# Kernel tuning notes

Hardware: AMD Instinct MI355X
Metric: run time of the kernel (lower is better)

Reference implementation:

```python
import jax, jax.numpy as jnp
import numpy as np

EMBED = 1024
DMODEL = 1024
NHEAD = 16
HEAD = DMODEL // NHEAD  # 64
EPS = 1e-5


def layer_norm(x, g, b):
    mu = jnp.mean(x, axis=-1, keepdims=True)
    var = jnp.var(x, axis=-1, keepdims=True)
    return (x - mu) / jnp.sqrt(var + EPS) * g + b


def setup_inputs() -> dict:
    key = jax.random.key(0)
    ks = jax.random.split(key, 16)
    s = 0.02
    B, T = 2, 2048
    return {
        "x": jax.random.normal(ks[0], (B, T, EMBED), jnp.float32),
        "wq": jax.random.normal(ks[1], (NHEAD, EMBED, HEAD), jnp.float32) * s,
        "bq": jnp.zeros((NHEAD, HEAD), jnp.float32),
        "wk": jax.random.normal(ks[2], (NHEAD, EMBED, HEAD), jnp.float32) * s,
        "bk": jnp.zeros((NHEAD, HEAD), jnp.float32),
        "wv": jax.random.normal(ks[3], (NHEAD, EMBED, HEAD), jnp.float32) * s,
        "bv": jnp.zeros((NHEAD, HEAD), jnp.float32),
        "ln1_g": jnp.ones((EMBED,), jnp.float32),
        "ln1_b": jnp.zeros((EMBED,), jnp.float32),
        "ln2_g": jnp.ones((DMODEL,), jnp.float32),
        "ln2_b": jnp.zeros((DMODEL,), jnp.float32),
        "w1": jax.random.normal(ks[4], (DMODEL, 4 * DMODEL), jnp.float32) * s,
        "b1": jnp.zeros((4 * DMODEL,), jnp.float32),
        "w2": jax.random.normal(ks[5], (4 * DMODEL, EMBED), jnp.float32) * s,
        "b2": jnp.zeros((EMBED,), jnp.float32),
    }


def reference(x, wq, bq, wk, bk, wv, bv, ln1_g, ln1_b, ln2_g, ln2_b, w1, b1, w2, b2):
    B, T, C = x.shape
    h = layer_norm(x, ln1_g, ln1_b)  # note: residual uses the normalized x (as in source)
    # per-head projections, vectorized over heads: [B,H,T,D]
    q = jnp.einsum('btc,hcd->bhtd', h, wq) + bq[None, :, None, :]
    k = jnp.einsum('btc,hcd->bhtd', h, wk) + bk[None, :, None, :]
    v = jnp.einsum('btc,hcd->bhtd', h, wv) + bv[None, :, None, :]
    scores = jnp.einsum('bhtd,bhsd->bhts', q, k) / jnp.sqrt(jnp.float32(HEAD))
    causal = jnp.tril(jnp.ones((T, T), bool))
    scores = jnp.where(causal[None, None], scores, jnp.finfo(scores.dtype).min)
    wei = jax.nn.softmax(scores, axis=-1)
    attn = jnp.einsum('bhts,bhsd->bhtd', wei, v)
    attn = attn.transpose(0, 2, 1, 3).reshape(B, T, NHEAD * HEAD)  # concat heads
    y = h + attn
    z = layer_norm(y, ln2_g, ln2_b)
    ff = jax.nn.relu(z @ w1 + b1) @ w2 + b2
    return z + ff
```

## Files before the change

kernel.cpp:

```cpp
#include <hip/hip_runtime.h>
#include <hip/hip_bf16.h>
#include <cstdint>
#include <cstddef>

typedef __attribute__((ext_vector_type(8))) short bf16x8;
typedef __attribute__((ext_vector_type(4))) float f32x4;
typedef __attribute__((ext_vector_type(4))) short short4v;
typedef __attribute__((ext_vector_type(2))) unsigned int uint2v;

__device__ inline void gload_lds16(const void* g, void* l) {
  __builtin_amdgcn_global_load_lds((const __attribute__((address_space(1))) void*)g,
                                   (__attribute__((address_space(3))) void*)l, 16, 0, 0);
}

__device__ inline float exp2_fast(float x) {
  float r;
  asm volatile("v_exp_f32 %0, %1" : "=v"(r) : "v"(x));
  return r;
}

__device__ inline unsigned int cvt_pk_bf16(float lo, float hi) {
  unsigned int r;
  asm volatile("v_cvt_pk_bf16_f32 %0, %1, %2" : "=v"(r) : "v"(lo), "v"(hi));
  return r;
}

__global__ void transpose_pack(const float* __restrict__ src, __hip_bfloat16* __restrict__ dst,
                               int R, int C, int ldDst, long zSrcStride, int zDstRow)
{
  __shared__ float tile[64][65];
  src += (size_t)blockIdx.z * zSrcStride;
  const int r0 = blockIdx.y * 64, c0 = blockIdx.x * 64;
  const int t = threadIdx.x;
#pragma unroll
  for (int i = 0; i < 16; ++i) {
    int idx = i * 256 + t;
    int r = idx >> 6, c = idx & 63;
    tile[r][c] = src[(size_t)(r0 + r) * C + c0 + c];
  }
  __syncthreads();
  const int drow0 = blockIdx.z * zDstRow + c0;
#pragma unroll
  for (int i = 0; i < 16; ++i) {
    int idx = i * 256 + t;
    int cc = idx >> 6, rr = idx & 63;
    dst[(size_t)(drow0 + cc) * ldDst + r0 + rr] = __float2bfloat16(tile[rr][cc]);
  }
}

__global__ void ln_fused(const float* __restrict__ x, const float* __restrict__ add,
                         const float* __restrict__ g, const float* __restrict__ bta,
                         float* __restrict__ of32, __hip_bfloat16* __restrict__ obf)
{
  const int row = blockIdx.x;
  const int t = threadIdx.x;
  float4 v = ((const float4*)(x + (size_t)row * 1024))[t];
  if (add) {
    float4 a = ((const float4*)(add + (size_t)row * 1024))[t];
    v.x += a.x; v.y += a.y; v.z += a.z; v.w += a.w;
  }
  float s = v.x + v.y + v.z + v.w;
  float ss = v.x * v.x + v.y * v.y + v.z * v.z + v.w * v.w;
#pragma unroll
  for (int off = 1; off < 64; off <<= 1) {
    s += __shfl_xor(s, off);
    ss += __shfl_xor(ss, off);
  }
  __shared__ float sb[4], ssb[4];
  const int w = t >> 6, lane = t & 63;
  if (lane == 0) { sb[w] = s; ssb[w] = ss; }
  __syncthreads();
  s = sb[0] + sb[1] + sb[2] + sb[3];
  ss = ssb[0] + ssb[1] + ssb[2] + ssb[3];
  const float mu = s * (1.f / 1024.f);
  const float var = ss * (1.f / 1024.f) - mu * mu;
  const float rstd = rsqrtf(var + 1e-5f);
  float4 gv = ((const float4*)g)[t];
  float4 bv = ((const float4*)bta)[t];
  float4 o;
  o.x = (v.x - mu) * rstd * gv.x + bv.x;
  o.y = (v.y - mu) * rstd * gv.y + bv.y;
  o.z = (v.z - mu) * rstd * gv.z + bv.z;
  o.w = (v.w - mu) * rstd * gv.w + bv.w;
  ((float4*)(of32 + (size_t)row * 1024))[t] = o;
  __hip_bfloat16 hb[4] = { __float2bfloat16(o.x), __float2bfloat16(o.y),
                           __float2bfloat16(o.z), __float2bfloat16(o.w) };
  *(short4v*)(obf + (size_t)row * 1024 + t * 4) = *(const short4v*)hb;
}

template<int EPI>
__global__ __launch_bounds__(512, 2) void gemm_bt(
    const __hip_bfloat16* __restrict__ A, const __hip_bfloat16* __restrict__ Bt,
    int N, int Kf, int kLen,
    const float* __restrict__ bias,
    const float* __restrict__ bq, const float* __restrict__ bk, const float* __restrict__ bv,
    __hip_bfloat16* __restrict__ oq, __hip_bfloat16* __restrict__ ok, __hip_bfloat16* __restrict__ ovt,
    __hip_bfloat16* __restrict__ obf,
    float* __restrict__ opart0, float* __restrict__ opart1, float* __restrict__ opart2)
{
  __shared__ short As[2][128 * 32];
  __shared__ short Bs[2][256 * 32];
  const int t = threadIdx.x;
  const int lane = t & 63;
  const int w = t >> 6;
  const int wm = w >> 2, wn = w & 3;
  const int l15 = lane & 15, lg = lane >> 4;
  const int m0 = blockIdx.y * 128;
  const int n0 = blockIdx.x * 256;
  const int kBase = (EPI == 2) ? (int)blockIdx.z * kLen : 0;
  const int kEnd0 = kBase + kLen;
  const int kEnd = (kEnd0 > Kf) ? Kf : kEnd0;

  f32x4 acc[4][4];
#pragma unroll
  for (int i = 0; i < 4; ++i)
#pragma unroll
    for (int j = 0; j < 4; ++j)
#pragma unroll
      for (int e = 0; e < 4; ++e) acc[i][j][e] = 0.f;

  auto STAGE = [&](int buf, int kk0) {
    {
      const int r = t >> 2, cc = t & 3;
      const int kk = (cc ^ ((r >> 1) & 3)) * 8;
      gload_lds16(A + (size_t)(m0 + r) * Kf + kk0 + kk, (char*)As + buf * 8192 + t * 16);
    }
#pragma unroll
    for (int i = 0; i < 2; ++i) {
      const int c = t + 512 * i;
      const int r = c >> 2, cc = c & 3;
      const int kk = (cc ^ ((r >> 1) & 3)) * 8;
      gload_lds16(Bt + (size_t)(n0 + r) * Kf + kk0 + kk, (char*)Bs + buf * 16384 + c * 16);
    }
  };

  STAGE(0, kBase);
  int buf = 0;
  for (int k0 = kBase; k0 < kEnd; k0 += 32) {
    const int knext = (k0 + 32 < kEnd) ? k0 + 32 : k0;
    STAGE(buf ^ 1, knext);
    asm volatile("s_waitcnt vmcnt(3)" ::: "memory");
    __builtin_amdgcn_s_barrier();
    asm volatile("" ::: "memory");

    bf16x8 af[4], bfr[4];
#pragma unroll
    for (int fm = 0; fm < 4; ++fm) {
      const int r = wm * 64 + fm * 16 + l15;
      const int kc = lg ^ ((r >> 1) & 3);
      af[fm] = *(const bf16x8*)&As[buf][r * 32 + kc * 8];
    }
#pragma unroll
    for (int fn = 0; fn < 4; ++fn) {
      const int r = wn * 64 + fn * 16 + l15;
      const int kc = lg ^ ((r >> 1) & 3);
      bfr[fn] = *(const bf16x8*)&Bs[buf][r * 32 + kc * 8];
    }
#pragma unroll
    for (int fm = 0; fm < 4; ++fm)
#pragma unroll
      for (int fn = 0; fn < 4; ++fn)
        acc[fm][fn] = __builtin_amdgcn_mfma_f32_16x16x32_bf16(af[fm], bfr[fn], acc[fm][fn], 0, 0, 0);

    asm volatile("" ::: "memory");
    __builtin_amdgcn_s_barrier();
    buf ^= 1;
  }

#pragma unroll
  for (int fm = 0; fm < 4; ++fm) {
    const int mbase = m0 + wm * 64 + fm * 16 + lg * 4;
#pragma unroll
    for (int fn = 0; fn < 4; ++fn) {
      const int n = n0 + wn * 64 + fn * 16 + l15;
      if (EPI == 0) {
        const int seg = n >> 10;
        const int cn = n & 1023;
        const int h = cn >> 6, d = cn & 63;
        const float* bp = (seg == 0) ? bq : (seg == 1) ? bk : bv;
        const float bias_v = bp[cn];
#pragma unroll
        for (int rg = 0; rg < 4; ++rg) {
          const int m = mbase + rg;
          const int b = m >> 11, tt = m & 2047;
          const size_t bh = (size_t)(b * 16 + h);
          const float val = acc[fm][fn][rg] + bias_v;
          if (seg == 0)      oq[(bh * 2048 + tt) * 64 + d] = __float2bfloat16(val);
          else if (seg == 1) ok[(bh * 2048 + tt) * 64 + d] = __float2bfloat16(val);
          else               ovt[(bh * 64 + d) * 2048 + tt] = __float2bfloat16(val);
        }
      } else if (EPI == 1) {
        const float bias_v = bias[n];
#pragma unroll
        for (int rg = 0; rg < 4; ++rg) {
          const int m = mbase + rg;
          float val = acc[fm][fn][rg] + bias_v;
          val = fmaxf(val, 0.f);
          obf[(size_t)m * N + n] = __float2bfloat16(val);
        }
      } else {
        float* op = (blockIdx.z == 0) ? opart0 : (blockIdx.z == 1) ? opart1 : opart2;
#pragma unroll
        for (int rg = 0; rg < 4; ++rg) {
          const int m = mbase + rg;
          op[(size_t)m * 1024 + n] = acc[fm][fn][rg];
        }
      }
    }
  }
}

__global__ void ffn2_merge(const float* __restrict__ p0, const float* __restrict__ p1,
                           const float* __restrict__ p2,
                           const float* __restrict__ z, const float* __restrict__ b2,
                           float* __restrict__ out)
{
  const size_t i = ((size_t)blockIdx.x * 256 + threadIdx.x) * 4;
  const float4 a = *(const float4*)(p0 + i);
  const float4 b = *(const float4*)(p1 + i);
  const float4 d = *(const float4*)(p2 + i);
  const float4 c = *(const float4*)(z + i);
  const float4 bb = *(const float4*)(b2 + (i & 1023));
  float4 o;
  o.x = c.x + bb.x + a.x + b.x + d.x;
  o.y = c.y + bb.y + a.y + b.y + d.y;
  o.z = c.z + bb.z + a.z + b.z + d.z;
  o.w = c.w + bb.w + a.w + b.w + d.w;
  *(float4*)(out + i) = o;
}

__global__ __launch_bounds__(256, 3) void flash_attn(
    const __hip_bfloat16* __restrict__ Q, const __hip_bfloat16* __restrict__ Kb,
    const __hip_bfloat16* __restrict__ Vt,
    __hip_bfloat16* __restrict__ Opart, float* __restrict__ Lpart)
{
  __shared__ short Ks[2][64 * 64];
  __shared__ short Vs[2][64 * 64];
  __shared__ short P2[4][32 * 72];
  const int t = threadIdx.x;
  const int lane = t & 63, w = t >> 6;
  const int l15 = lane & 15, lg = lane >> 4;
  const int chunk = blockIdx.x, qblk = blockIdx.y, bh = blockIdx.z;
  const int q0 = qblk * 128;
  const int s_base = chunk * 512;
  if (s_base > q0 + 127) return;
  const int s_hi = (s_base + 512 < q0 + 128) ? s_base + 512 : q0 + 128;
  const int ntiles = (s_hi - s_base) >> 6;
  const int qw = q0 + w * 32;

  const __hip_bfloat16* Qbh = Q + (size_t)bh * 2048 * 64;
  const __hip_bfloat16* Kbh = Kb + (size_t)bh * 2048 * 64;
  const __hip_bfloat16* Vbh = Vt + (size_t)bh * 64 * 2048;

  bf16x8 qf[2][2];
#pragma unroll
  for (int fm = 0; fm < 2; ++fm)
#pragma unroll
    for (int kc = 0; kc < 2; ++kc)
      qf[fm][kc] = *(const bf16x8*)(Qbh + (size_t)(qw + fm * 16 + l15) * 64 + kc * 32 + lg * 8);

  const int srow = (w << 4) + (lane >> 3);
  const int schunk = ((lane & 7) ^ (lane >> 3)) * 8;

  auto STAGE = [&](int bufi, int s0) {
#pragma unroll
    for (int i = 0; i < 2; ++i) {
      const int r = srow + i * 8;
      const int dst = bufi * 8192 + w * 2048 + i * 1024 + lane * 16;
      gload_lds16(Kbh + (size_t)(s0 + r) * 64 + schunk, (char*)Ks + dst);
      gload_lds16(Vbh + (size_t)r * 2048 + s0 + schunk, (char*)Vs + dst);
    }
  };

  f32x4 o_acc[2][4];
  float lpart[2] = {0.f, 0.f};
#pragma unroll
  for (int fm = 0; fm < 2; ++fm)
#pragma unroll
    for (int fd = 0; fd < 4; ++fd)
#pragma unroll
      for (int e = 0; e < 4; ++e) o_acc[fm][fd][e] = 0.f;

  const float C = 0.18033688011112042f;

  STAGE(0, s_base);
  int cur = 0;
  for (int ti = 0; ti < ntiles; ++ti) {
    const int s0 = s_base + ti * 64;
    const int nxt = (ti + 1 < ntiles) ? s0 + 64 : s0;
    STAGE(cur ^ 1, nxt);
    asm volatile("s_waitcnt vmcnt(4)" ::: "memory");
    __builtin_amdgcn_s_barrier();
    asm volatile("" ::: "memory");

    if (s0 <= qw + 31) {
      f32x4 s_acc[2][4];
#pragma unroll
      for (int fm = 0; fm < 2; ++fm)
#pragma unroll
        for (int fn = 0; fn < 4; ++fn)
#pragma unroll
          for (int e = 0; e < 4; ++e) s_acc[fm][fn][e] = 0.f;
#pragma unroll
      for (int kc = 0; kc < 2; ++kc)
#pragma unroll
        for (int fn = 0; fn < 4; ++fn) {
          const int r = fn * 16 + l15;
          bf16x8 kf = *(const bf16x8*)&Ks[cur][r * 64 + ((((kc << 2) | lg) ^ (l15 & 7)) << 3)];
          s_acc[0][fn] = __builtin_amdgcn_mfma_f32_16x16x32_bf16(kf, qf[0][kc], s_acc[0][fn], 0, 0, 0);
          s_acc[1][fn] = __builtin_amdgcn_mfma_f32_16x16x32_bf16(kf, qf[1][kc], s_acc[1][fn], 0, 0, 0);
        }

      const bool needmask = (s0 + 63 > qw);
      float pr[2][4][4];
#pragma unroll
      for (int fm = 0; fm < 2; ++fm) {
        const int qv = qw + fm * 16 + l15;
#pragma unroll
        for (int fn = 0; fn < 4; ++fn)
#pragma unroll
          for (int rg = 0; rg < 4; ++rg) {
            float p = exp2_fast(s_acc[fm][fn][rg] * C);
            if (needmask) {
              const int sg = s0 + fn * 16 + lg * 4 + rg;
              p = (sg <= qv) ? p : 0.f;
            }
            pr[fm][fn][rg] = p;
            lpart[fm] += p;
          }
      }

#pragma unroll
      for (int fm = 0; fm < 2; ++fm)
#pragma unroll
        for (int fn = 0; fn < 4; ++fn) {
          uint2v u;
          u.x = cvt_pk_bf16(pr[fm][fn][0], pr[fm][fn][1]);
          u.y = cvt_pk_bf16(pr[fm][fn][2], pr[fm][fn][3]);
          *(uint2v*)&P2[w][(fm * 16 + l15) * 72 + fn * 16 + lg * 4] = u;
        }

#pragma unroll
      for (int kc = 0; kc < 2; ++kc) {
        bf16x8 pf0 = *(const bf16x8*)&P2[w][(l15) * 72 + kc * 32 + lg * 8];
        bf16x8 pf1 = *(const bf16x8*)&P2[w][(16 + l15) * 72 + kc * 32 + lg * 8];
#pragma unroll
        for (int fd = 0; fd < 4; ++fd) {
          const int r = fd * 16 + l15;
          bf16x8 vf = *(const bf16x8*)&Vs[cur][r * 64 + ((((kc << 2) | lg) ^ (l15 & 7)) << 3)];
          o_acc[0][fd] = __builtin_amdgcn_mfma_f32_16x16x32_bf16(vf, pf0, o_acc[0][fd], 0, 0, 0);
          o_acc[1][fd] = __builtin_amdgcn_mfma_f32_16x16x32_bf16(vf, pf1, o_acc[1][fd], 0, 0, 0);
        }
      }
    }

    asm volatile("" ::: "memory");
    __builtin_amdgcn_s_barrier();
    cur ^= 1;
  }

  const int pslot = ((bh * 16 + qblk) << 2) + chunk;
  __hip_bfloat16* op = Opart + (size_t)pslot * 8192;
#pragma unroll
  for (int fm = 0; fm < 2; ++fm) {
    float l = lpart[fm];
    l += __shfl_xor(l, 16);
    l += __shfl_xor(l, 32);
    const int qloc = w * 32 + fm * 16 + l15;
    if (lg == 0) Lpart[pslot * 128 + qloc] = l;
#pragma unroll
    for (int fd = 0; fd < 4; ++fd) {
      uint2v u;
      u.x = cvt_pk_bf16(o_acc[fm][fd][0], o_acc[fm][fd][1]);
      u.y = cvt_pk_bf16(o_acc[fm][fd][2], o_acc[fm][fd][3]);
      *(uint2v*)(op + (size_t)qloc * 64 + fd * 16 + lg * 4) = u;
    }
  }
}

__global__ void flash_merge(const __hip_bfloat16* __restrict__ Opart,
                            const float* __restrict__ Lpart, float* __restrict__ attn)
{
  const int qblk = blockIdx.x, bh = blockIdx.y;
  const int b = bh >> 4, h = bh & 15;
  const int nch = (qblk >> 2) + 1;
  const int t = threadIdx.x;
  const int r = t >> 1, half = t & 1;
  const int base = (bh * 16 + qblk) << 2;

  float l = 0.f;
  float o[32];
#pragma unroll
  for (int j = 0; j < 32; ++j) o[j] = 0.f;

  for (int ch = 0; ch < nch; ++ch) {
    l += Lpart[(base + ch) * 128 + r];
    const __hip_bfloat16* op = Opart + (size_t)(base + ch) * 8192 + r * 64 + half * 32;
#pragma unroll
    for (int j = 0; j < 4; ++j) {
      bf16x8 v = *(const bf16x8*)(op + j * 8);
#pragma unroll
      for (int e = 0; e < 8; ++e) {
        unsigned int bits = ((unsigned int)(unsigned short)v[e]) << 16;
        o[j * 8 + e] += __uint_as_float(bits);
      }
    }
  }
  const float inv = 1.f / l;
  float* dst = attn + (size_t)(b * 2048 + qblk * 128 + r) * 1024 + h * 64 + half * 32;
#pragma unroll
  for (int j = 0; j < 8; ++j) {
    float4 v4;
    v4.x = o[j * 4 + 0] * inv; v4.y = o[j * 4 + 1] * inv;
    v4.z = o[j * 4 + 2] * inv; v4.w = o[j * 4 + 3] * inv;
    ((float4*)dst)[j] = v4;
  }
}

extern "C" void kernel_launch(void* const* d_in, const int* in_sizes, int n_in,
                              void* d_out, int out_size, void* d_ws, size_t ws_size,
                              hipStream_t stream) {
  const float* x    = (const float*)d_in[0];
  const float* wq   = (const float*)d_in[1];
  const float* bq   = (const float*)d_in[2];
  const float* wk   = (const float*)d_in[3];
  const float* bk   = (const float*)d_in[4];
  const float* wv   = (const float*)d_in[5];
  const float* bv   = (const float*)d_in[6];
  const float* ln1g = (const float*)d_in[7];
  const float* ln1b = (const float*)d_in[8];
  const float* ln2g = (const float*)d_in[9];
  const float* ln2b = (const float*)d_in[10];
  const float* w1   = (const float*)d_in[11];
  const float* b1   = (const float*)d_in[12];
  const float* w2   = (const float*)d_in[13];
  const float* b2   = (const float*)d_in[14];
  float* out = (float*)d_out;

  char* ws = (char*)d_ws;
  const size_t MB = 1024 * 1024;
  __hip_bfloat16* h_bf  = (__hip_bfloat16*)(ws + 0);
  float* Lpart          = (float*)(ws + 0);
  __hip_bfloat16* qb    = (__hip_bfloat16*)(ws + 8 * MB);
  __hip_bfloat16* kb    = (__hip_bfloat16*)(ws + 16 * MB);
  __hip_bfloat16* vtb   = (__hip_bfloat16*)(ws + 24 * MB);
  __hip_bfloat16* ff1   = (__hip_bfloat16*)(ws + 0);
  float* h_f32          = (float*)(ws + 32 * MB);
  float* p0             = (float*)(ws + 32 * MB);
  float* attn           = (float*)(ws + 48 * MB);
  float* p1             = (float*)(ws + 48 * MB);
  __hip_bfloat16* Opart = (__hip_bfloat16*)(ws + 64 * MB);
  float* z_f32          = (float*)(ws + 64 * MB);
  __hip_bfloat16* z_bf  = (__hip_bfloat16*)(ws + 80 * MB);
  __hip_bfloat16* wqkvT = (__hip_bfloat16*)(ws + 88 * MB);
  float* p2             = (float*)(ws + 88 * MB);
  __hip_bfloat16* w1T   = (__hip_bfloat16*)(ws + 96 * MB);
  __hip_bfloat16* w2T   = (__hip_bfloat16*)(ws + 104 * MB);

  transpose_pack<<<dim3(1, 16, 16), 256, 0, stream>>>(wq, wqkvT + 0 * 1024 * 1024, 1024, 64, 1024, 65536, 64);
  transpose_pack<<<dim3(1, 16, 16), 256, 0, stream>>>(wk, wqkvT + 1 * 1024 * 1024, 1024, 64, 1024, 65536, 64);
  transpose_pack<<<dim3(1, 16, 16), 256, 0, stream>>>(wv, wqkvT + 2 * 1024 * 1024, 1024, 64, 1024, 65536, 64);
  transpose_pack<<<dim3(64, 16, 1), 256, 0, stream>>>(w1, w1T, 1024, 4096, 1024, 0, 0);
  transpose_pack<<<dim3(16, 64, 1), 256, 0, stream>>>(w2, w2T, 4096, 1024, 4096, 0, 0);

  ln_fused<<<4096, 256, 0, stream>>>(x, nullptr, ln1g, ln1b, h_f32, h_bf);

  gemm_bt<0><<<dim3(12, 32), 512, 0, stream>>>(h_bf, wqkvT, 3072, 1024, 1024,
      nullptr, bq, bk, bv, qb, kb, vtb, nullptr, nullptr, nullptr, nullptr);

  flash_attn<<<dim3(4, 16, 32), 256, 0, stream>>>(qb, kb, vtb, Opart, Lpart);
  flash_merge<<<dim3(16, 32), 256, 0, stream>>>(Opart, Lpart, attn);

  ln_fused<<<4096, 256, 0, stream>>>(h_f32, attn, ln2g, ln2b, z_f32, z_bf);

  gemm_bt<1><<<dim3(16, 32), 512, 0, stream>>>(z_bf, w1T, 4096, 1024, 1024,
      b1, nullptr, nullptr, nullptr, nullptr, nullptr, nullptr, ff1, nullptr, nullptr, nullptr);

  gemm_bt<2><<<dim3(4, 32, 3), 512, 0, stream>>>(ff1, w2T, 1024, 4096, 1376,
      nullptr, nullptr, nullptr, nullptr, nullptr, nullptr, nullptr, nullptr, p0, p1, p2);

  ffn2_merge<<<4096, 256, 0, stream>>>(p0, p1, p2, z_f32, b2, out);
}
```

Before: 258.3 us.

## Read K and V fragments directly from global memory in flash attention

Removes the double-buffered LDS staging of K and V tiles, along with the block barriers, in the flash attention kernel. Each wave now loads its MFMA K/V fragments straight from global memory (relying on L1/L2 caching) and exits the tile loop early once past the causal limit. This cuts LDS usage and synchronisation, but each of the four waves now fetches the same K/V data redundantly and loses the async prefetch overlap.

```diff
diff --git a/kernel.cpp b/kernel.cpp
--- a/kernel.cpp
+++ b/kernel.cpp
@@ -234,8 +234,6 @@
     const __hip_bfloat16* __restrict__ Vt,
     __hip_bfloat16* __restrict__ Opart, float* __restrict__ Lpart)
 {
-  __shared__ short Ks[2][64 * 64];
-  __shared__ short Vs[2][64 * 64];
   __shared__ short P2[4][32 * 72];
   const int t = threadIdx.x;
   const int lane = t & 63, w = t >> 6;
@@ -259,19 +257,6 @@
     for (int kc = 0; kc < 2; ++kc)
       qf[fm][kc] = *(const bf16x8*)(Qbh + (size_t)(qw + fm * 16 + l15) * 64 + kc * 32 + lg * 8);
 
-  const int srow = (w << 4) + (lane >> 3);
-  const int schunk = ((lane & 7) ^ (lane >> 3)) * 8;
-
-  auto STAGE = [&](int bufi, int s0) {
-#pragma unroll
-    for (int i = 0; i < 2; ++i) {
-      const int r = srow + i * 8;
-      const int dst = bufi * 8192 + w * 2048 + i * 1024 + lane * 16;
-      gload_lds16(Kbh + (size_t)(s0 + r) * 64 + schunk, (char*)Ks + dst);
-      gload_lds16(Vbh + (size_t)r * 2048 + s0 + schunk, (char*)Vs + dst);
-    }
-  };
-
   f32x4 o_acc[2][4];
   float lpart[2] = {0.f, 0.f};
 #pragma unroll
@@ -283,80 +268,66 @@
 
   const float C = 0.18033688011112042f;
 
-  STAGE(0, s_base);
-  int cur = 0;
   for (int ti = 0; ti < ntiles; ++ti) {
     const int s0 = s_base + ti * 64;
-    const int nxt = (ti + 1 < ntiles) ? s0 + 64 : s0;
-    STAGE(cur ^ 1, nxt);
-    asm volatile("s_waitcnt vmcnt(4)" ::: "memory");
-    __builtin_amdgcn_s_barrier();
-    asm volatile("" ::: "memory");
-
-    if (s0 <= qw + 31) {
-      f32x4 s_acc[2][4];
-#pragma unroll
-      for (int fm = 0; fm < 2; ++fm)
-#pragma unroll
-        for (int fn = 0; fn < 4; ++fn)
-#pragma unroll
-          for (int e = 0; e < 4; ++e) s_acc[fm][fn][e] = 0.f;
-#pragma unroll
-      for (int kc = 0; kc < 2; ++kc)
-#pragma unroll
-        for (int fn = 0; fn < 4; ++fn) {
-          const int r = fn * 16 + l15;
-          bf16x8 kf = *(const bf16x8*)&Ks[cur][r * 64 + ((((kc << 2) | lg) ^ (l15 & 7)) << 3)];
-          s_acc[0][fn] = __builtin_amdgcn_mfma_f32_16x16x32_bf16(kf, qf[0][kc], s_acc[0][fn], 0, 0, 0);
-          s_acc[1][fn] = __builtin_amdgcn_mfma_f32_16x16x32_bf16(kf, qf[1][kc], s_acc[1][fn], 0, 0, 0);
+    if (s0 > qw + 31) break;
+
+    f32x4 s_acc[2][4];
+#pragma unroll
+    for (int fm = 0; fm < 2; ++fm)
+#pragma unroll
+      for (int fn = 0; fn < 4; ++fn)
+#pragma unroll
+        for (int e = 0; e < 4; ++e) s_acc[fm][fn][e] = 0.f;
+#pragma unroll
+    for (int kc = 0; kc < 2; ++kc)
+#pragma unroll
+      for (int fn = 0; fn < 4; ++fn) {
+        bf16x8 kf = *(const bf16x8*)(Kbh + (size_t)(s0 + fn * 16 + l15) * 64 + kc * 32 + lg * 8);
+        s_acc[0][fn] = __builtin_amdgcn_mfma_f32_16x16x32_bf16(kf, qf[0][kc], s_acc[0][fn], 0, 0, 0);
+        s_acc[1][fn] = __builtin_amdgcn_mfma_f32_16x16x32_bf16(kf, qf[1][kc], s_acc[1][fn], 0, 0, 0);
+      }
+
+    const bool needmask = (s0 + 63 > qw);
+    float pr[2][4][4];
+#pragma unroll
+    for (int fm = 0; fm < 2; ++fm) {
+      const int qv = qw + fm * 16 + l15;
+#pragma unroll
+      for (int fn = 0; fn < 4; ++fn)
+#pragma unroll
+        for (int rg = 0; rg < 4; ++rg) {
+          float p = exp2_fast(s_acc[fm][fn][rg] * C);
+          if (needmask) {
+            const int sg = s0 + fn * 16 + lg * 4 + rg;
+            p = (sg <= qv) ? p : 0.f;
+          }
+          pr[fm][fn][rg] = p;
+          lpart[fm] += p;
         }
-
-      const bool needmask = (s0 + 63 > qw);
-      float pr[2][4][4];
-#pragma unroll
-      for (int fm = 0; fm < 2; ++fm) {
-        const int qv = qw + fm * 16 + l15;
-#pragma unroll
-        for (int fn = 0; fn < 4; ++fn)
-#pragma unroll
-          for (int rg = 0; rg < 4; ++rg) {
-            float p = exp2_fast(s_acc[fm][fn][rg] * C);
-            if (needmask) {
-              const int sg = s0 + fn * 16 + lg * 4 + rg;
-              p = (sg <= qv) ? p : 0.f;
-            }
-            pr[fm][fn][rg] = p;
-            lpart[fm] += p;
-          }
+    }
+
+#pragma unroll
+    for (int fm = 0; fm < 2; ++fm)
+#pragma unroll
+      for (int fn = 0; fn < 4; ++fn) {
+        uint2v u;
+        u.x = cvt_pk_bf16(pr[fm][fn][0], pr[fm][fn][1]);
+        u.y = cvt_pk_bf16(pr[fm][fn][2], pr[fm][fn][3]);
+        *(uint2v*)&P2[w][(fm * 16 + l15) * 72 + fn * 16 + lg * 4] = u;
       }
 
 #pragma unroll
-      for (int fm = 0; fm < 2; ++fm)
-#pragma unroll
-        for (int fn = 0; fn < 4; ++fn) {
-          uint2v u;
-          u.x = cvt_pk_bf16(pr[fm][fn][0], pr[fm][fn][1]);
-          u.y = cvt_pk_bf16(pr[fm][fn][2], pr[fm][fn][3]);
-          *(uint2v*)&P2[w][(fm * 16 + l15) * 72 + fn * 16 + lg * 4] = u;
-        }
-
-#pragma unroll
-      for (int kc = 0; kc < 2; ++kc) {
-        bf16x8 pf0 = *(const bf16x8*)&P2[w][(l15) * 72 + kc * 32 + lg * 8];
-        bf16x8 pf1 = *(const bf16x8*)&P2[w][(16 + l15) * 72 + kc * 32 + lg * 8];
-#pragma unroll
-        for (int fd = 0; fd < 4; ++fd) {
-          const int r = fd * 16 + l15;
-          bf16x8 vf = *(const bf16x8*)&Vs[cur][r * 64 + ((((kc << 2) | lg) ^ (l15 & 7)) << 3)];
-          o_acc[0][fd] = __builtin_amdgcn_mfma_f32_16x16x32_bf16(vf, pf0, o_acc[0][fd], 0, 0, 0);
-          o_acc[1][fd] = __builtin_amdgcn_mfma_f32_16x16x32_bf16(vf, pf1, o_acc[1][fd], 0, 0, 0);
-        }
+    for (int kc = 0; kc < 2; ++kc) {
+      bf16x8 pf0 = *(const bf16x8*)&P2[w][(l15) * 72 + kc * 32 + lg * 8];
+      bf16x8 pf1 = *(const bf16x8*)&P2[w][(16 + l15) * 72 + kc * 32 + lg * 8];
+#pragma unroll
+      for (int fd = 0; fd < 4; ++fd) {
+        bf16x8 vf = *(const bf16x8*)(Vbh + (size_t)(fd * 16 + l15) * 2048 + s0 + kc * 32 + lg * 8);
+        o_acc[0][fd] = __builtin_amdgcn_mfma_f32_16x16x32_bf16(vf, pf0, o_acc[0][fd], 0, 0, 0);
+        o_acc[1][fd] = __builtin_amdgcn_mfma_f32_16x16x32_bf16(vf, pf1, o_acc[1][fd], 0, 0, 0);
       }
     }
-
-    asm volatile("" ::: "memory");
-    __builtin_amdgcn_s_barrier();
-    cur ^= 1;
   }
 
   const int pslot = ((bh * 16 + qblk) << 2) + chunk;
```

Result: slower. 325.9 us (+26.2%).
